# Performance work log

Hardware: AMD Instinct MI355X
Metric: run time of the kernel (lower is better)

The kernel has to match this reference:

```python
import jax, jax.numpy as jnp
import numpy as np

N_NODES = 100000
N_EDGES = 1600000
D_FEAT = 64


def setup_inputs() -> dict:
    key = jax.random.key(0)
    k1, k2, k3, k4 = jax.random.split(key, 4)
    rows = jax.random.randint(k1, (N_EDGES,), 0, N_NODES, dtype=jnp.int32)
    cols = jax.random.randint(k2, (N_EDGES,), 0, N_NODES, dtype=jnp.int32)
    vals = jax.random.uniform(k3, (N_EDGES,), dtype=jnp.float32)
    embeds = jax.random.normal(k4, (N_NODES, D_FEAT), dtype=jnp.float32)
    return {"rows": rows, "cols": cols, "vals": vals, "embeds": embeds,
            "n_nodes": N_NODES}


def reference(rows, cols, vals, embeds, n_nodes):
    # GCN sparse aggregation: res[i] = sum_{e: rows[e]==i} vals[e] * embeds[cols[e]]
    # Equivalent to adj.matmul(embeds) with adj in COO form.
    msgs = vals[:, None] * embeds[cols]            # [E, D] gather + scale
    res = jax.ops.segment_sum(msgs, rows, num_segments=n_nodes)  # [N, D] scatter-add
    return res
```

## Files before the change

### kernel.cpp

```cpp
#include <hip/hip_runtime.h>
#include <hip/hip_bf16.h>


#define D_FEAT 64
#define LOG_RPB 7
#define ROWS_PER_BUCKET 128
#define N_BUCKETS 782
#define PB 256
#define K1_CAP 6272
#define K4_CAP 3072

typedef unsigned long long u64;

__global__ __launch_bounds__(256) void gcn_scatter_fallback(
    const int* __restrict__ rows, const int* __restrict__ cols,
    const float* __restrict__ vals, const float* __restrict__ embeds,
    float* __restrict__ out, int n_edges)
{
    int gtid = blockIdx.x * blockDim.x + threadIdx.x;
    int e = gtid >> 4;
    if (e >= n_edges) return;
    int lane4 = gtid & 15;
    int row = rows[e]; int col = cols[e]; float v = vals[e];
    const float4* ep = reinterpret_cast<const float4*>(embeds + (size_t)col * D_FEAT);
    float4 m = ep[lane4];
    float* op = out + (size_t)row * D_FEAT + lane4 * 4;
    atomicAdd(op + 0, v * m.x);
    atomicAdd(op + 1, v * m.y);
    atomicAdd(op + 2, v * m.z);
    atomicAdd(op + 3, v * m.w);
}

__device__ inline int wave_incl_scan(int x, int lane) {
    #pragma unroll
    for (int o = 1; o < 64; o <<= 1) {
        int y = __shfl_up(x, o, 64);
        if (lane >= o) x += y;
    }
    return x;
}

__global__ __launch_bounds__(512) void k_partition_sort(
    const int* __restrict__ rows, const int* __restrict__ cols,
    const float* __restrict__ vals, u64* __restrict__ sorted,
    int* __restrict__ offg, int n_edges, int chunk)
{
    __shared__ u64 ebuf[K1_CAP];
    __shared__ int lh[N_BUCKETS];
    __shared__ int cur[N_BUCKETS];
    __shared__ int segtot[16];

    int blk = blockIdx.x, tid = threadIdx.x;
    int lane = tid & 63, wid = tid >> 6;
    int beg = blk * chunk;
    int end = min(beg + chunk, n_edges);
    int cnt = end - beg;

    for (int i = tid; i < N_BUCKETS; i += 512) lh[i] = 0;
    __syncthreads();
    for (int e = beg + tid; e < end; e += 512)
        atomicAdd(&lh[rows[e] >> LOG_RPB], 1);
    __syncthreads();

    for (int seg = wid; seg * 64 < N_BUCKETS; seg += 8) {
        int idx = seg * 64 + lane;
        int v = (idx < N_BUCKETS) ? lh[idx] : 0;
        int inc = wave_incl_scan(v, lane);
        if (idx < N_BUCKETS) lh[idx] = inc - v;
        if (lane == 63) segtot[seg] = inc;
    }
    __syncthreads();
    if (tid < 64) {
        int v = (tid < 13) ? segtot[tid] : 0;
        int inc = wave_incl_scan(v, tid);
        if (tid < 13) segtot[tid] = inc - v;
    }
    __syncthreads();
    int* myoff = offg + (size_t)blk * (N_BUCKETS + 1);
    for (int i = tid; i < N_BUCKETS; i += 512) {
        int excl = lh[i] + segtot[i >> 6];
        myoff[i] = excl;
        cur[i] = excl;
    }
    if (tid == 0) myoff[N_BUCKETS] = cnt;
    __syncthreads();

    for (int e = beg + tid; e < end; e += 512) {
        int r = rows[e];
        int b = r >> LOG_RPB;
        unsigned meta = (unsigned)cols[e] |
                        ((unsigned)(r & (ROWS_PER_BUCKET - 1)) << 17);
        u64 ent = ((u64)__float_as_uint(vals[e]) << 32) | meta;
        int p = atomicAdd(&cur[b], 1);
        ebuf[p] = ent;
    }
    __syncthreads();

    for (int i = tid; i < cnt; i += 512)
        sorted[beg + i] = ebuf[i];
}

__global__ __launch_bounds__(512) void k_aggregate_seg(
    const u64* __restrict__ sorted, const int* __restrict__ offg,
    const float* __restrict__ embeds, float* __restrict__ out,
    int n_nodes, int chunk)
{
    __shared__ u64 ebuf[K4_CAP];
    __shared__ int sOff[PB], sLen[PB], sBase[PB];
    __shared__ int wtot[8];
    __shared__ int rcnt[ROWS_PER_BUCKET];
    __shared__ int roff[ROWS_PER_BUCKET + 1];
    __shared__ int rcur[ROWS_PER_BUCKET];

    int b = blockIdx.x, tid = threadIdx.x;
    int lane = tid & 63, wid = tid >> 6;
    int rowbase = b * ROWS_PER_BUCKET;
    int nrows = n_nodes - rowbase;
    if (nrows > ROWS_PER_BUCKET) nrows = ROWS_PER_BUCKET;

    if (tid < PB) {
        int o0 = offg[(size_t)tid * (N_BUCKETS + 1) + b];
        int o1 = offg[(size_t)tid * (N_BUCKETS + 1) + b + 1];
        sOff[tid] = o0;
        sLen[tid] = o1 - o0;
    }
    for (int i = tid; i < ROWS_PER_BUCKET; i += 512) rcnt[i] = 0;
    __syncthreads();

    if (wid < 4) {
        int v = sLen[wid * 64 + lane];
        int inc = wave_incl_scan(v, lane);
        sBase[wid * 64 + lane] = inc - v;
        if (lane == 63) wtot[wid] = inc;
    }
    __syncthreads();
    if (tid < PB) {
        int c = 0;
        for (int w = 0; w < (tid >> 6); ++w) c += wtot[w];
        sBase[tid] += c;
    }
    int n = wtot[0] + wtot[1] + wtot[2] + wtot[3];
    __syncthreads();

    if (n <= K4_CAP) {
        for (int g = wid; g < PB / 8; g += 8) {
            int seg = g * 8 + (lane >> 3);
            int len = sLen[seg];
            const u64* sp = sorted + (size_t)seg * chunk + sOff[seg];
            for (int i = (lane & 7); i < len; i += 8)
                atomicAdd(&rcnt[(int)((sp[i] >> 17) & (ROWS_PER_BUCKET - 1))], 1);
        }
        __syncthreads();

        if (tid < 64) {
            int a = rcnt[tid], c = rcnt[64 + tid];
            int ia = wave_incl_scan(a, tid);
            int ta = __shfl(ia, 63, 64);
            int ic = wave_incl_scan(c, tid);
            int ea = ia - a;
            int ec = ta + ic - c;
            roff[tid] = ea;       rcur[tid] = ea;
            roff[64 + tid] = ec;  rcur[64 + tid] = ec;
            if (tid == 63) roff[ROWS_PER_BUCKET] = ta + __shfl(ic, 63, 64);
        }
        __syncthreads();

        for (int g = wid; g < PB / 8; g += 8) {
            int seg = g * 8 + (lane >> 3);
            int len = sLen[seg];
            const u64* sp = sorted + (size_t)seg * chunk + sOff[seg];
            for (int i = (lane & 7); i < len; i += 8) {
                u64 ent = sp[i];
                int lr = (int)((ent >> 17) & (ROWS_PER_BUCKET - 1));
                int p = atomicAdd(&rcur[lr], 1);
                ebuf[p] = ent;
            }
        }
        __syncthreads();

        for (int lr = wid; lr < ROWS_PER_BUCKET; lr += 8) {
            int rs = roff[lr], re = roff[lr + 1];
            float acc = 0.0f;
            int j = rs;
            for (; j + 7 < re; j += 8) {
                u64 t0 = ebuf[j + 0], t1 = ebuf[j + 1], t2 = ebuf[j + 2], t3 = ebuf[j + 3];
                u64 t4 = ebuf[j + 4], t5 = ebuf[j + 5], t6 = ebuf[j + 6], t7 = ebuf[j + 7];
                float m0 = embeds[(size_t)(t0 & 0x1FFFF) * D_FEAT + lane];
                float m1 = embeds[(size_t)(t1 & 0x1FFFF) * D_FEAT + lane];
                float m2 = embeds[(size_t)(t2 & 0x1FFFF) * D_FEAT + lane];
                float m3 = embeds[(size_t)(t3 & 0x1FFFF) * D_FEAT + lane];
                float m4 = embeds[(size_t)(t4 & 0x1FFFF) * D_FEAT + lane];
                float m5 = embeds[(size_t)(t5 & 0x1FFFF) * D_FEAT + lane];
                float m6 = embeds[(size_t)(t6 & 0x1FFFF) * D_FEAT + lane];
                float m7 = embeds[(size_t)(t7 & 0x1FFFF) * D_FEAT + lane];
                acc += __uint_as_float((unsigned)(t0 >> 32)) * m0;
                acc += __uint_as_float((unsigned)(t1 >> 32)) * m1;
                acc += __uint_as_float((unsigned)(t2 >> 32)) * m2;
                acc += __uint_as_float((unsigned)(t3 >> 32)) * m3;
                acc += __uint_as_float((unsigned)(t4 >> 32)) * m4;
                acc += __uint_as_float((unsigned)(t5 >> 32)) * m5;
                acc += __uint_as_float((unsigned)(t6 >> 32)) * m6;
                acc += __uint_as_float((unsigned)(t7 >> 32)) * m7;
            }
            for (; j + 3 < re; j += 4) {
                u64 t0 = ebuf[j + 0], t1 = ebuf[j + 1], t2 = ebuf[j + 2], t3 = ebuf[j + 3];
                float m0 = embeds[(size_t)(t0 & 0x1FFFF) * D_FEAT + lane];
                float m1 = embeds[(size_t)(t1 & 0x1FFFF) * D_FEAT + lane];
                float m2 = embeds[(size_t)(t2 & 0x1FFFF) * D_FEAT + lane];
                float m3 = embeds[(size_t)(t3 & 0x1FFFF) * D_FEAT + lane];
                acc += __uint_as_float((unsigned)(t0 >> 32)) * m0;
                acc += __uint_as_float((unsigned)(t1 >> 32)) * m1;
                acc += __uint_as_float((unsigned)(t2 >> 32)) * m2;
                acc += __uint_as_float((unsigned)(t3 >> 32)) * m3;
            }
            for (; j < re; ++j) {
                u64 t0 = ebuf[j];
                acc += __uint_as_float((unsigned)(t0 >> 32)) *
                       embeds[(size_t)(t0 & 0x1FFFF) * D_FEAT + lane];
            }
            if (lr < nrows)
                out[(size_t)(rowbase + lr) * D_FEAT + lane] = acc;
        }
    } else {
        for (int i = tid; i < nrows * D_FEAT; i += 512)
            out[(size_t)rowbase * D_FEAT + i] = 0.0f;
        __syncthreads();
        for (int seg = wid; seg < PB; seg += 8) {
            int len = sLen[seg];
            const u64* sp = sorted + (size_t)seg * chunk + sOff[seg];
            for (int i = 0; i < len; ++i) {
                u64 ent = sp[i];
                int lr = (int)((ent >> 17) & (ROWS_PER_BUCKET - 1));
                int c = (int)(ent & 0x1FFFF);
                float v = __uint_as_float((unsigned)(ent >> 32));
                float m = embeds[(size_t)c * D_FEAT + lane];
                atomicAdd(&out[(size_t)(rowbase + lr) * D_FEAT + lane], v * m);
            }
        }
    }
}

extern "C" void kernel_launch(void* const* d_in, const int* in_sizes, int n_in,
                              void* d_out, int out_size, void* d_ws, size_t ws_size,
                              hipStream_t stream) {
    const int*   rows   = (const int*)d_in[0];
    const int*   cols   = (const int*)d_in[1];
    const float* vals   = (const float*)d_in[2];
    const float* embeds = (const float*)d_in[3];

    float* out = (float*)d_out;
    int n_edges = in_sizes[0];
    int n_nodes = out_size / D_FEAT;
    int n_buckets = (n_nodes + ROWS_PER_BUCKET - 1) >> LOG_RPB;
    int chunk = (n_edges + PB - 1) / PB;

    size_t need = (size_t)n_edges * sizeof(u64) +
                  (size_t)PB * (N_BUCKETS + 1) * sizeof(int) + 256;

    if (n_buckets != N_BUCKETS || chunk > K1_CAP || ws_size < need) {
        hipMemsetAsync(out, 0, (size_t)out_size * sizeof(float), stream);
        long long total_threads = (long long)n_edges * 16;
        int block = 256;
        int grid = (int)((total_threads + block - 1) / block);
        gcn_scatter_fallback<<<grid, block, 0, stream>>>(rows, cols, vals, embeds, out, n_edges);
        return;
    }

    u64* sorted = (u64*)d_ws;
    int* offg   = (int*)(sorted + n_edges);

    k_partition_sort<<<PB, 512, 0, stream>>>(rows, cols, vals, sorted, offg,
                                             n_edges, chunk);
    k_aggregate_seg<<<N_BUCKETS, 512, 0, stream>>>(sorted, offg, embeds, out,
                                                   n_nodes, chunk);
}
```

Measured before the change: 167.0 us.

## Gather bf16-converted embeddings and double partition blocks

Adds a pre-pass that rounds the fp32 embedding table to bf16 in workspace, and has the aggregation kernel gather 16-bit values that it widens to fp32 before accumulating. This halves the bytes moved by the random gathers. The partition kernel now runs 512 blocks of 256 threads with half-size chunks, and the aggregation kernel's segment scans are adjusted for the larger segment count. The cost is precision loss from bf16 inputs, an extra conversion kernel reading and writing the table on every call, and twice as many segment offsets to read per bucket.

```diff
diff --git a/kernel.cpp b/kernel.cpp
--- a/kernel.cpp
+++ b/kernel.cpp
@@ -6,8 +6,8 @@
 #define LOG_RPB 7
 #define ROWS_PER_BUCKET 128
 #define N_BUCKETS 782
-#define PB 256
-#define K1_CAP 6272
+#define PB 512
+#define K1_CAP 3136
 #define K4_CAP 3072
 
 typedef unsigned long long u64;
@@ -40,7 +40,19 @@
     return x;
 }
 
-__global__ __launch_bounds__(512) void k_partition_sort(
+__global__ __launch_bounds__(256) void k_convert(
+    const float* __restrict__ src, unsigned short* __restrict__ dst, int n)
+{
+    int i = blockIdx.x * 256 + threadIdx.x;
+    int stride = gridDim.x * 256;
+    for (; i < n; i += stride) {
+        unsigned u = __float_as_uint(src[i]);
+        unsigned r = (u + 0x7FFFu + ((u >> 16) & 1u)) >> 16;
+        dst[i] = (unsigned short)r;
+    }
+}
+
+__global__ __launch_bounds__(256) void k_partition_sort(
     const int* __restrict__ rows, const int* __restrict__ cols,
     const float* __restrict__ vals, u64* __restrict__ sorted,
     int* __restrict__ offg, int n_edges, int chunk)
@@ -56,13 +68,13 @@
     int end = min(beg + chunk, n_edges);
     int cnt = end - beg;
 
-    for (int i = tid; i < N_BUCKETS; i += 512) lh[i] = 0;
-    __syncthreads();
-    for (int e = beg + tid; e < end; e += 512)
+    for (int i = tid; i < N_BUCKETS; i += 256) lh[i] = 0;
+    __syncthreads();
+    for (int e = beg + tid; e < end; e += 256)
         atomicAdd(&lh[rows[e] >> LOG_RPB], 1);
     __syncthreads();
 
-    for (int seg = wid; seg * 64 < N_BUCKETS; seg += 8) {
+    for (int seg = wid; seg * 64 < N_BUCKETS; seg += 4) {
         int idx = seg * 64 + lane;
         int v = (idx < N_BUCKETS) ? lh[idx] : 0;
         int inc = wave_incl_scan(v, lane);
@@ -77,7 +89,7 @@
     }
     __syncthreads();
     int* myoff = offg + (size_t)blk * (N_BUCKETS + 1);
-    for (int i = tid; i < N_BUCKETS; i += 512) {
+    for (int i = tid; i < N_BUCKETS; i += 256) {
         int excl = lh[i] + segtot[i >> 6];
         myoff[i] = excl;
         cur[i] = excl;
@@ -85,7 +97,7 @@
     if (tid == 0) myoff[N_BUCKETS] = cnt;
     __syncthreads();
 
-    for (int e = beg + tid; e < end; e += 512) {
+    for (int e = beg + tid; e < end; e += 256) {
         int r = rows[e];
         int b = r >> LOG_RPB;
         unsigned meta = (unsigned)cols[e] |
@@ -96,14 +108,15 @@
     }
     __syncthreads();
 
-    for (int i = tid; i < cnt; i += 512)
+    for (int i = tid; i < cnt; i += 256)
         sorted[beg + i] = ebuf[i];
 }
 
+template <bool USE16>
 __global__ __launch_bounds__(512) void k_aggregate_seg(
     const u64* __restrict__ sorted, const int* __restrict__ offg,
-    const float* __restrict__ embeds, float* __restrict__ out,
-    int n_nodes, int chunk)
+    const float* __restrict__ embeds, const unsigned short* __restrict__ emb16,
+    float* __restrict__ out, int n_nodes, int chunk)
 {
     __shared__ u64 ebuf[K4_CAP];
     __shared__ int sOff[PB], sLen[PB], sBase[PB];
@@ -127,27 +140,28 @@
     for (int i = tid; i < ROWS_PER_BUCKET; i += 512) rcnt[i] = 0;
     __syncthreads();
 
-    if (wid < 4) {
+    {
         int v = sLen[wid * 64 + lane];
         int inc = wave_incl_scan(v, lane);
         sBase[wid * 64 + lane] = inc - v;
         if (lane == 63) wtot[wid] = inc;
     }
     __syncthreads();
-    if (tid < PB) {
+    {
         int c = 0;
-        for (int w = 0; w < (tid >> 6); ++w) c += wtot[w];
-        sBase[tid] += c;
-    }
-    int n = wtot[0] + wtot[1] + wtot[2] + wtot[3];
+        for (int w = 0; w < wid; ++w) c += wtot[w];
+        sBase[wid * 64 + lane] += c;
+    }
+    int n = 0;
+    for (int w = 0; w < 8; ++w) n += wtot[w];
     __syncthreads();
 
     if (n <= K4_CAP) {
-        for (int g = wid; g < PB / 8; g += 8) {
-            int seg = g * 8 + (lane >> 3);
+        for (int g = wid; g < PB / 16; g += 8) {
+            int seg = g * 16 + (lane >> 2);
             int len = sLen[seg];
             const u64* sp = sorted + (size_t)seg * chunk + sOff[seg];
-            for (int i = (lane & 7); i < len; i += 8)
+            for (int i = (lane & 3); i < len; i += 4)
                 atomicAdd(&rcnt[(int)((sp[i] >> 17) & (ROWS_PER_BUCKET - 1))], 1);
         }
         __syncthreads();
@@ -165,11 +179,11 @@
         }
         __syncthreads();
 
-        for (int g = wid; g < PB / 8; g += 8) {
-            int seg = g * 8 + (lane >> 3);
+        for (int g = wid; g < PB / 16; g += 8) {
+            int seg = g * 16 + (lane >> 2);
             int len = sLen[seg];
             const u64* sp = sorted + (size_t)seg * chunk + sOff[seg];
-            for (int i = (lane & 7); i < len; i += 8) {
+            for (int i = (lane & 3); i < len; i += 4) {
                 u64 ent = sp[i];
                 int lr = (int)((ent >> 17) & (ROWS_PER_BUCKET - 1));
                 int p = atomicAdd(&rcur[lr], 1);
@@ -182,17 +196,14 @@
             int rs = roff[lr], re = roff[lr + 1];
             float acc = 0.0f;
             int j = rs;
+            #define GATHER(t) (USE16 \
+                ? __uint_as_float((unsigned)emb16[(size_t)((t) & 0x1FFFF) * D_FEAT + lane] << 16) \
+                : embeds[(size_t)((t) & 0x1FFFF) * D_FEAT + lane])
             for (; j + 7 < re; j += 8) {
                 u64 t0 = ebuf[j + 0], t1 = ebuf[j + 1], t2 = ebuf[j + 2], t3 = ebuf[j + 3];
                 u64 t4 = ebuf[j + 4], t5 = ebuf[j + 5], t6 = ebuf[j + 6], t7 = ebuf[j + 7];
-                float m0 = embeds[(size_t)(t0 & 0x1FFFF) * D_FEAT + lane];
-                float m1 = embeds[(size_t)(t1 & 0x1FFFF) * D_FEAT + lane];
-                float m2 = embeds[(size_t)(t2 & 0x1FFFF) * D_FEAT + lane];
-                float m3 = embeds[(size_t)(t3 & 0x1FFFF) * D_FEAT + lane];
-                float m4 = embeds[(size_t)(t4 & 0x1FFFF) * D_FEAT + lane];
-                float m5 = embeds[(size_t)(t5 & 0x1FFFF) * D_FEAT + lane];
-                float m6 = embeds[(size_t)(t6 & 0x1FFFF) * D_FEAT + lane];
-                float m7 = embeds[(size_t)(t7 & 0x1FFFF) * D_FEAT + lane];
+                float m0 = GATHER(t0), m1 = GATHER(t1), m2 = GATHER(t2), m3 = GATHER(t3);
+                float m4 = GATHER(t4), m5 = GATHER(t5), m6 = GATHER(t6), m7 = GATHER(t7);
                 acc += __uint_as_float((unsigned)(t0 >> 32)) * m0;
                 acc += __uint_as_float((unsigned)(t1 >> 32)) * m1;
                 acc += __uint_as_float((unsigned)(t2 >> 32)) * m2;
@@ -204,10 +215,7 @@
             }
             for (; j + 3 < re; j += 4) {
                 u64 t0 = ebuf[j + 0], t1 = ebuf[j + 1], t2 = ebuf[j + 2], t3 = ebuf[j + 3];
-                float m0 = embeds[(size_t)(t0 & 0x1FFFF) * D_FEAT + lane];
-                float m1 = embeds[(size_t)(t1 & 0x1FFFF) * D_FEAT + lane];
-                float m2 = embeds[(size_t)(t2 & 0x1FFFF) * D_FEAT + lane];
-                float m3 = embeds[(size_t)(t3 & 0x1FFFF) * D_FEAT + lane];
+                float m0 = GATHER(t0), m1 = GATHER(t1), m2 = GATHER(t2), m3 = GATHER(t3);
                 acc += __uint_as_float((unsigned)(t0 >> 32)) * m0;
                 acc += __uint_as_float((unsigned)(t1 >> 32)) * m1;
                 acc += __uint_as_float((unsigned)(t2 >> 32)) * m2;
@@ -215,9 +223,9 @@
             }
             for (; j < re; ++j) {
                 u64 t0 = ebuf[j];
-                acc += __uint_as_float((unsigned)(t0 >> 32)) *
-                       embeds[(size_t)(t0 & 0x1FFFF) * D_FEAT + lane];
-            }
+                acc += __uint_as_float((unsigned)(t0 >> 32)) * GATHER(t0);
+            }
+            #undef GATHER
             if (lr < nrows)
                 out[(size_t)(rowbase + lr) * D_FEAT + lane] = acc;
         }
@@ -254,10 +262,11 @@
     int n_buckets = (n_nodes + ROWS_PER_BUCKET - 1) >> LOG_RPB;
     int chunk = (n_edges + PB - 1) / PB;
 
-    size_t need = (size_t)n_edges * sizeof(u64) +
-                  (size_t)PB * (N_BUCKETS + 1) * sizeof(int) + 256;
-
-    if (n_buckets != N_BUCKETS || chunk > K1_CAP || ws_size < need) {
+    size_t base_need = (size_t)n_edges * sizeof(u64) +
+                       (size_t)PB * (N_BUCKETS + 1) * sizeof(int) + 256;
+    size_t full_need = base_need + (size_t)n_nodes * D_FEAT * sizeof(unsigned short) + 256;
+
+    if (n_buckets != N_BUCKETS || chunk > K1_CAP || ws_size < base_need) {
         hipMemsetAsync(out, 0, (size_t)out_size * sizeof(float), stream);
         long long total_threads = (long long)n_edges * 16;
         int block = 256;
@@ -268,9 +277,20 @@
 
     u64* sorted = (u64*)d_ws;
     int* offg   = (int*)(sorted + n_edges);
-
-    k_partition_sort<<<PB, 512, 0, stream>>>(rows, cols, vals, sorted, offg,
+    unsigned short* emb16 = (unsigned short*)
+        (((uintptr_t)(offg + (size_t)PB * (N_BUCKETS + 1)) + 15) & ~(uintptr_t)15);
+
+    bool use16 = (ws_size >= full_need);
+
+    if (use16)
+        k_convert<<<512, 256, 0, stream>>>(embeds, emb16, n_nodes * D_FEAT);
+
+    k_partition_sort<<<PB, 256, 0, stream>>>(rows, cols, vals, sorted, offg,
                                              n_edges, chunk);
-    k_aggregate_seg<<<N_BUCKETS, 512, 0, stream>>>(sorted, offg, embeds, out,
-                                                   n_nodes, chunk);
-}
+    if (use16)
+        k_aggregate_seg<true><<<N_BUCKETS, 512, 0, stream>>>(
+            sorted, offg, embeds, emb16, out, n_nodes, chunk);
+    else
+        k_aggregate_seg<false><<<N_BUCKETS, 512, 0, stream>>>(
+            sorted, offg, embeds, emb16, out, n_nodes, chunk);
+}
```

Result: no change. 166.9 us (-0.1%).
